# Kernel tuning notes

Hardware: AMD Instinct MI355X
Metric: run time of the kernel (lower is better)

## Reference

```python
import jax, jax.numpy as jnp
import numpy as np

N, E, F, H, C = 50000, 800000, 128, 256, 40
BN_EPS = 1e-5


def setup_inputs() -> dict:
    key = jax.random.key(0)
    ks = jax.random.split(key, 8)
    s = 0.05
    return {
        'x': jax.random.normal(ks[0], (N, F), jnp.float32),
        'edge_index': jax.random.randint(ks[1], (2, E), 0, N),
        'eps1': jnp.zeros((), jnp.float32),
        'W1': jax.random.normal(ks[2], (F, H), jnp.float32) * s,
        'b1': jnp.zeros((H,), jnp.float32),
        'g1': jnp.ones((H,), jnp.float32),
        'be1': jnp.zeros((H,), jnp.float32),
        'W2': jax.random.normal(ks[3], (H, H), jnp.float32) * s,
        'b2': jnp.zeros((H,), jnp.float32),
        'eps2': jnp.zeros((), jnp.float32),
        'W3': jax.random.normal(ks[4], (H, H), jnp.float32) * s,
        'b3': jnp.zeros((H,), jnp.float32),
        'g2': jnp.ones((H,), jnp.float32),
        'be2': jnp.zeros((H,), jnp.float32),
        'W4': jax.random.normal(ks[5], (H, H), jnp.float32) * s,
        'b4': jnp.zeros((H,), jnp.float32),
        'g3': jnp.ones((H,), jnp.float32),
        'be3': jnp.zeros((H,), jnp.float32),
        'Wf': jax.random.normal(ks[6], (H, C), jnp.float32) * s,
        'bf': jnp.zeros((C,), jnp.float32),
    }


def _bn(h, g, b):
    # BatchNorm1d forward with batch statistics (training-mode math, biased var)
    m = jnp.mean(h, axis=0)
    v = jnp.var(h, axis=0)
    return (h - m) * jax.lax.rsqrt(v + BN_EPS) * g + b


def _gin_conv(x, edge_index, eps, Wa, ba, g, be, Wb, bb):
    # GINConv: out = mlp((1+eps)*x + sum_{(src->dst)} x[src])
    src, dst = edge_index[0], edge_index[1]
    agg = jax.ops.segment_sum(x[src], dst, num_segments=x.shape[0])  # [N, d]
    h = (1.0 + eps) * x + agg
    h = jnp.maximum(_bn(h @ Wa + ba, g, be), 0.0)  # Linear-BN-ReLU
    return h @ Wb + bb                              # Linear


def reference(x, edge_index, eps1, W1, b1, g1, be1, W2, b2,
              eps2, W3, b3, g2, be2, W4, b4, g3, be3, Wf, bf):
    h = _gin_conv(x, edge_index, eps1, W1, b1, g1, be1, W2, b2)
    h = jnp.maximum(h, 0.0)  # F.relu (dropout p=0)
    h = _gin_conv(h, edge_index, eps2, W3, b3, g2, be2, W4, b4)
    h = jnp.maximum(_bn(h, g3, be3), 0.0)  # bn2 + relu
    return h @ Wf + bf  # fc -> [N, C]
```

## Files before the change

### kernel.cpp

```cpp
#include <hip/hip_runtime.h>
#include <hip/hip_bf16.h>


#define NN 50000
#define EE 800000
#define FDIM 128
#define HDIM 256
#define CDIM 40
#define BN_EPS 1e-5f
#define CSTRIDE 136

typedef unsigned short u16;
typedef unsigned int u32;
typedef __attribute__((ext_vector_type(8))) short short8;
typedef __attribute__((ext_vector_type(4))) float f32x4;

__device__ __forceinline__ float bflo(u32 u) { return __uint_as_float(u << 16); }
__device__ __forceinline__ float bfhi(u32 u) { return __uint_as_float(u & 0xFFFF0000u); }
__device__ __forceinline__ u16 f2bf(float f) {
  __hip_bfloat16 h = __float2bfloat16(f);
  return *(u16*)&h;
}
__device__ __forceinline__ u32 pack2(float a, float b) {
  return (u32)f2bf(a) | ((u32)f2bf(b) << 16);
}

__global__ void k_hist(const int* __restrict__ ei, int* __restrict__ deg) {
  int e = blockIdx.x * 256 + threadIdx.x;
  if (e < EE) atomicAdd(&deg[ei[EE + e]], 1);
}

__global__ void k_scan_blocks(const int* __restrict__ in, int* __restrict__ partial,
                              int* __restrict__ bsums, int n) {
  __shared__ int s[256];
  int i = blockIdx.x * 256 + threadIdx.x;
  s[threadIdx.x] = (i < n) ? in[i] : 0;
  __syncthreads();
  for (int d = 1; d < 256; d <<= 1) {
    int t = (threadIdx.x >= d) ? s[threadIdx.x - d] : 0;
    __syncthreads();
    s[threadIdx.x] += t;
    __syncthreads();
  }
  if (i < n) partial[i] = s[threadIdx.x];
  if (threadIdx.x == 255) bsums[blockIdx.x] = s[255];
}

__global__ void k_scan_sums(int* __restrict__ bs, int nb) {
  __shared__ int s[256];
  s[threadIdx.x] = (threadIdx.x < nb) ? bs[threadIdx.x] : 0;
  __syncthreads();
  for (int d = 1; d < 256; d <<= 1) {
    int t = (threadIdx.x >= d) ? s[threadIdx.x - d] : 0;
    __syncthreads();
    s[threadIdx.x] += t;
    __syncthreads();
  }
  int ex = (threadIdx.x == 0) ? 0 : s[threadIdx.x - 1];
  if (threadIdx.x < nb) bs[threadIdx.x] = ex;
}

__global__ void k_scan_add(const int* __restrict__ partial, const int* __restrict__ bs,
                           int* __restrict__ rowstart, int n) {
  int i = blockIdx.x * 256 + threadIdx.x;
  if (i < n) rowstart[i + 1] = partial[i] + bs[blockIdx.x];
  if (i == 0) rowstart[0] = 0;
}

__global__ void k_copy_i32(const int* __restrict__ a, int* __restrict__ b, int n) {
  int i = blockIdx.x * 256 + threadIdx.x;
  if (i < n) b[i] = a[i];
}

__global__ void k_scatter(const int* __restrict__ ei, int* __restrict__ cursor,
                          int* __restrict__ sorted_src) {
  int e = blockIdx.x * 256 + threadIdx.x;
  if (e < EE) {
    int dst = ei[EE + e];
    int p = atomicAdd(&cursor[dst], 1);
    sorted_src[p] = ei[e];
  }
}

__global__ void k_cvt_x(const float* __restrict__ x, u16* __restrict__ xb) {
  int i = blockIdx.x * 256 + threadIdx.x;
  size_t base = (size_t)i * 4;
  if (base < (size_t)NN * FDIM) {
    float4 v = *(const float4*)&x[base];
    u32 lo = pack2(v.x, v.y), hi = pack2(v.z, v.w);
    *(uint2*)&xb[base] = make_uint2(lo, hi);
  }
}

__global__ void k_cvt_wt(const float* __restrict__ W, u16* __restrict__ Wt, int K) {
  int i = blockIdx.x * 256 + threadIdx.x;
  int k = i >> 8, n = i & 255;
  if (k < K) Wt[(size_t)n * K + k] = f2bf(W[i]);
}

template <int FEAT>
__global__ __launch_bounds__(256)
void k_agg(const u16* __restrict__ x, const int* __restrict__ rowstart,
           const int* __restrict__ sorted_src, const float* __restrict__ epsp,
           u16* __restrict__ out) {
  int node = blockIdx.x * 4 + (threadIdx.x >> 6);
  if (node >= NN) return;
  int lane = threadIdx.x & 63;
  float e1 = 1.0f + epsp[0];
  int s = rowstart[node], t = rowstart[node + 1];
  if constexpr (FEAT == 128) {
    const u32* xp = (const u32*)x;
    u32 u = xp[(size_t)node * 64 + lane];
    float a0 = bflo(u) * e1, a1 = bfhi(u) * e1;
    int p = s;
    for (; p + 7 < t; p += 8) {
      u32 uu[8];
#pragma unroll
      for (int i = 0; i < 8; ++i) uu[i] = xp[(size_t)sorted_src[p + i] * 64 + lane];
#pragma unroll
      for (int i = 0; i < 8; ++i) { a0 += bflo(uu[i]); a1 += bfhi(uu[i]); }
    }
    for (; p + 1 < t; p += 2) {
      u32 u0 = xp[(size_t)sorted_src[p] * 64 + lane];
      u32 u1 = xp[(size_t)sorted_src[p + 1] * 64 + lane];
      a0 += bflo(u0) + bflo(u1);
      a1 += bfhi(u0) + bfhi(u1);
    }
    if (p < t) {
      u32 u0 = xp[(size_t)sorted_src[p] * 64 + lane];
      a0 += bflo(u0); a1 += bfhi(u0);
    }
    ((u32*)out)[(size_t)node * 64 + lane] = pack2(a0, a1);
  } else {
    const uint2* xp = (const uint2*)x;
    uint2 u = xp[(size_t)node * 64 + lane];
    float a0 = bflo(u.x) * e1, a1 = bfhi(u.x) * e1;
    float a2 = bflo(u.y) * e1, a3 = bfhi(u.y) * e1;
    int p = s;
    for (; p + 7 < t; p += 8) {
      uint2 uu[8];
#pragma unroll
      for (int i = 0; i < 8; ++i) uu[i] = xp[(size_t)sorted_src[p + i] * 64 + lane];
#pragma unroll
      for (int i = 0; i < 8; ++i) {
        a0 += bflo(uu[i].x); a1 += bfhi(uu[i].x);
        a2 += bflo(uu[i].y); a3 += bfhi(uu[i].y);
      }
    }
    for (; p + 1 < t; p += 2) {
      uint2 u0 = xp[(size_t)sorted_src[p] * 64 + lane];
      uint2 u1 = xp[(size_t)sorted_src[p + 1] * 64 + lane];
      a0 += bflo(u0.x) + bflo(u1.x);
      a1 += bfhi(u0.x) + bfhi(u1.x);
      a2 += bflo(u0.y) + bflo(u1.y);
      a3 += bfhi(u0.y) + bfhi(u1.y);
    }
    if (p < t) {
      uint2 u0 = xp[(size_t)sorted_src[p] * 64 + lane];
      a0 += bflo(u0.x); a1 += bfhi(u0.x);
      a2 += bflo(u0.y); a3 += bfhi(u0.y);
    }
    ((uint2*)out)[(size_t)node * 64 + lane] = make_uint2(pack2(a0, a1), pack2(a2, a3));
  }
}

template <int K, bool TRANSFORM, bool RELU_OUT, bool COLSUMS>
__global__ __launch_bounds__(256)
void k_gemm(const u16* __restrict__ A, const u16* __restrict__ Bt,
            const float* __restrict__ bias, const float* __restrict__ ta,
            const float* __restrict__ tc, u16* __restrict__ C,
            float* __restrict__ csum, float* __restrict__ csq) {
  constexpr int NCH = K / 8;
  constexpr int NKS = K / 32;
  constexpr int NTILE = (NN + 31) / 32;
  __shared__ u16 Bs[128 * K];
  __shared__ u16 Cs[32 * CSTRIDE];
  __shared__ float2 Tb[K];

  const int tid = threadIdx.x;
  const int lane = tid & 63;
  const int w = tid >> 6;
  const int wm = w >> 1, wn = w & 1;
  const int lr = lane & 15, lq = lane >> 4;
  const int half = blockIdx.x & 1;
  const u16* Bth = Bt + (size_t)half * 128 * K;

  for (int i = tid; i < 128 * NCH; i += 256) {
    int row = i / NCH, c = i % NCH;
    short8 v = *(const short8*)&Bth[(size_t)row * K + c * 8];
    ((short8*)Bs)[row * NCH + (c ^ (row & 7))] = v;
  }
  if constexpr (TRANSFORM) {
    for (int k = tid; k < K; k += 256) Tb[k] = make_float2(ta[k], tc[k]);
  }

  float bv[4];
#pragma unroll
  for (int ni = 0; ni < 4; ++ni) bv[ni] = bias[half * 128 + wn * 64 + ni * 16 + lr];
  float colS[4] = {}, colQ[4] = {};

  __syncthreads();

  short8 bufA[NKS], bufB[NKS];

  auto LOADA = [&](short8* dst, int rt) {
    int row = rt * 32 + wm * 16 + lr;
    int rowc = row < NN ? row : NN - 1;
    const u16* Ap = &A[(size_t)rowc * K];
#pragma unroll
    for (int ks = 0; ks < NKS; ++ks)
      dst[ks] = *(const short8*)&Ap[ks * 32 + lq * 8];
  };

  auto BODY = [&](short8* cur, short8* nxt, int rt) {
    if constexpr (TRANSFORM) {
#pragma unroll
      for (int ks = 0; ks < NKS; ++ks) {
        short8 v = cur[ks];
#pragma unroll
        for (int j = 0; j < 8; ++j) {
          float2 tb = Tb[ks * 32 + lq * 8 + j];
          float f = __uint_as_float(((u32)(u16)v[j]) << 16);
          v[j] = (short)f2bf(fmaxf(fmaf(f, tb.x, tb.y), 0.f));
        }
        cur[ks] = v;
      }
    }
    if (rt + 256 < NTILE) LOADA(nxt, rt + 256);

    f32x4 acc[4];
#pragma unroll
    for (int ni = 0; ni < 4; ++ni) acc[ni] = (f32x4){0.f, 0.f, 0.f, 0.f};
    __builtin_amdgcn_s_setprio(1);
#pragma unroll
    for (int ks = 0; ks < NKS; ++ks) {
#pragma unroll
      for (int ni = 0; ni < 4; ++ni) {
        int col = wn * 64 + ni * 16 + lr;
        int c = (ks * 4 + lq) ^ (col & 7);
        short8 bfr = ((const short8*)Bs)[col * NCH + c];
        acc[ni] = __builtin_amdgcn_mfma_f32_16x16x32_bf16(cur[ks], bfr, acc[ni], 0, 0, 0);
      }
    }
    __builtin_amdgcn_s_setprio(0);

#pragma unroll
    for (int ni = 0; ni < 4; ++ni) {
      int col = wn * 64 + ni * 16 + lr;
#pragma unroll
      for (int j = 0; j < 4; ++j) {
        int r = wm * 16 + lq * 4 + j;
        float v = acc[ni][j] + bv[ni];
        if constexpr (RELU_OUT) v = fmaxf(v, 0.f);
        if constexpr (COLSUMS) {
          if (rt * 32 + r < NN) { colS[ni] += v; colQ[ni] += v * v; }
        }
        Cs[r * CSTRIDE + col] = f2bf(v);
      }
    }
    __syncthreads();
    {
      int r = tid >> 3;
      int gr = rt * 32 + r;
      if (gr < NN) {
        const uint4* src = (const uint4*)&Cs[r * CSTRIDE + (tid & 7) * 16];
        uint4 v0 = src[0], v1 = src[1];
        uint4* dst = (uint4*)&C[(size_t)gr * HDIM + half * 128 + (tid & 7) * 16];
        dst[0] = v0; dst[1] = v1;
      }
    }
    __syncthreads();
  };

  LOADA(bufA, blockIdx.x >> 1);
  for (int rt = blockIdx.x >> 1; rt < NTILE; rt += 512) {
    BODY(bufA, bufB, rt);
    if (rt + 256 < NTILE) BODY(bufB, bufA, rt + 256);
  }

  if constexpr (COLSUMS) {
#pragma unroll
    for (int ni = 0; ni < 4; ++ni) {
      float s = colS[ni], q = colQ[ni];
      s += __shfl_xor(s, 16); s += __shfl_xor(s, 32);
      q += __shfl_xor(q, 16); q += __shfl_xor(q, 32);
      if (lq == 0) {
        int col = half * 128 + wn * 64 + ni * 16 + lr;
        atomicAdd(&csum[col], s);
        atomicAdd(&csq[col], q);
      }
    }
  }
}

__global__ void k_bn_fin(const float* __restrict__ sum, const float* __restrict__ sq,
                         const float* __restrict__ g, const float* __restrict__ be,
                         float* __restrict__ a, float* __restrict__ c) {
  int t = threadIdx.x;
  float m = sum[t] * (1.0f / NN);
  float var = sq[t] * (1.0f / NN) - m * m;
  float s = g[t] * rsqrtf(var + BN_EPS);
  a[t] = s;
  c[t] = be[t] - m * s;
}

__global__ __launch_bounds__(256)
void k_gemm_final(const u16* __restrict__ A, const float* __restrict__ B,
                  const float* __restrict__ bias, const float* __restrict__ ta,
                  const float* __restrict__ tc, float* __restrict__ C) {
  __shared__ float As[64][65];
  __shared__ float Bs[64][CDIM];
  int tid = threadIdx.x;
  int r = tid & 63, q = tid >> 6;
  int r0 = blockIdx.x * 64;
  float acc[10] = {};
  for (int k0 = 0; k0 < HDIM; k0 += 64) {
#pragma unroll
    for (int i = 0; i < 4; ++i) {
      int idx = tid + i * 256;
      int row = idx >> 4;
      int c4 = (idx & 15) * 4;
      int gr = r0 + row;
      float v0 = 0.f, v1 = 0.f, v2 = 0.f, v3 = 0.f;
      if (gr < NN) {
        uint2 u = *(const uint2*)&A[(size_t)gr * HDIM + k0 + c4];
        v0 = fmaxf(fmaf(bflo(u.x), ta[k0 + c4 + 0], tc[k0 + c4 + 0]), 0.f);
        v1 = fmaxf(fmaf(bfhi(u.x), ta[k0 + c4 + 1], tc[k0 + c4 + 1]), 0.f);
        v2 = fmaxf(fmaf(bflo(u.y), ta[k0 + c4 + 2], tc[k0 + c4 + 2]), 0.f);
        v3 = fmaxf(fmaf(bfhi(u.y), ta[k0 + c4 + 3], tc[k0 + c4 + 3]), 0.f);
      }
      As[c4 + 0][row] = v0;
      As[c4 + 1][row] = v1;
      As[c4 + 2][row] = v2;
      As[c4 + 3][row] = v3;
    }
#pragma unroll
    for (int i = 0; i < 10; ++i) {
      int idx = tid + i * 256;
      int row = idx / CDIM;
      int col = idx % CDIM;
      Bs[row][col] = B[(size_t)(k0 + row) * CDIM + col];
    }
    __syncthreads();
#pragma unroll
    for (int k = 0; k < 64; ++k) {
      float a = As[k][r];
#pragma unroll
      for (int j = 0; j < 10; ++j) acc[j] = fmaf(a, Bs[k][q * 10 + j], acc[j]);
    }
    __syncthreads();
  }
  int gr = r0 + r;
  if (gr < NN) {
#pragma unroll
    for (int j = 0; j < 10; ++j) C[(size_t)gr * CDIM + q * 10 + j] = acc[j] + bias[q * 10 + j];
  }
}

extern "C" void kernel_launch(void* const* d_in, const int* in_sizes, int n_in,
                              void* d_out, int out_size, void* d_ws, size_t ws_size,
                              hipStream_t stream) {
  const float* x   = (const float*)d_in[0];
  const int*   ei  = (const int*)d_in[1];
  const float* eps1= (const float*)d_in[2];
  const float* W1  = (const float*)d_in[3];
  const float* b1  = (const float*)d_in[4];
  const float* g1  = (const float*)d_in[5];
  const float* be1 = (const float*)d_in[6];
  const float* W2  = (const float*)d_in[7];
  const float* b2  = (const float*)d_in[8];
  const float* eps2= (const float*)d_in[9];
  const float* W3  = (const float*)d_in[10];
  const float* b3  = (const float*)d_in[11];
  const float* g2  = (const float*)d_in[12];
  const float* be2 = (const float*)d_in[13];
  const float* W4  = (const float*)d_in[14];
  const float* b4  = (const float*)d_in[15];
  const float* g3  = (const float*)d_in[16];
  const float* be3 = (const float*)d_in[17];
  const float* Wf  = (const float*)d_in[18];
  const float* bf  = (const float*)d_in[19];
  float* out = (float*)d_out;

  char* p = (char*)d_ws;
  auto alloc = [&](size_t bytes) -> char* {
    char* r = p;
    p += (bytes + 255) & ~(size_t)255;
    return r;
  };
  float* stats   = (float*)alloc(12 * 256 * sizeof(float));
  int* deg       = (int*)alloc(NN * sizeof(int));
  int* rowstart  = (int*)alloc((NN + 16) * sizeof(int));
  int* cursor    = (int*)alloc(NN * sizeof(int));
  int* sorted    = (int*)alloc(EE * sizeof(int));
  int* partial   = (int*)alloc(NN * sizeof(int));
  int* bsums     = (int*)alloc(1024 * sizeof(int));
  u16* W1t       = (u16*)alloc(256 * 128 * sizeof(u16));
  u16* W2t       = (u16*)alloc(256 * 256 * sizeof(u16));
  u16* W3t       = (u16*)alloc(256 * 256 * sizeof(u16));
  u16* W4t       = (u16*)alloc(256 * 256 * sizeof(u16));
  u16* xb        = (u16*)alloc((size_t)NN * 128 * sizeof(u16));
  u16* A1        = (u16*)alloc((size_t)NN * 128 * sizeof(u16));
  u16* z1        = (u16*)alloc((size_t)NN * 256 * sizeof(u16));
  u16* h1        = (u16*)alloc((size_t)NN * 256 * sizeof(u16));
  u16* A2        = (u16*)alloc((size_t)NN * 256 * sizeof(u16));
  (void)alloc(64 * 1024);
  u16* z2 = z1;
  u16* z3 = h1;

  hipMemsetAsync(deg, 0, NN * sizeof(int), stream);
  hipMemsetAsync(stats, 0, 12 * 256 * sizeof(float), stream);

  const int nbE = (EE + 255) / 256;
  const int nbN = (NN + 255) / 256;

  k_hist<<<nbE, 256, 0, stream>>>(ei, deg);
  k_scan_blocks<<<nbN, 256, 0, stream>>>(deg, partial, bsums, NN);
  k_scan_sums<<<1, 256, 0, stream>>>(bsums, nbN);
  k_scan_add<<<nbN, 256, 0, stream>>>(partial, bsums, rowstart, NN);
  k_copy_i32<<<nbN, 256, 0, stream>>>(rowstart, cursor, NN);
  k_scatter<<<nbE, 256, 0, stream>>>(ei, cursor, sorted);

  k_cvt_x<<<(NN * FDIM / 4 + 255) / 256, 256, 0, stream>>>(x, xb);
  k_cvt_wt<<<128, 256, 0, stream>>>(W1, W1t, 128);
  k_cvt_wt<<<256, 256, 0, stream>>>(W2, W2t, 256);
  k_cvt_wt<<<256, 256, 0, stream>>>(W3, W3t, 256);
  k_cvt_wt<<<256, 256, 0, stream>>>(W4, W4t, 256);

  k_agg<128><<<(NN + 3) / 4, 256, 0, stream>>>(xb, rowstart, sorted, eps1, A1);
  k_gemm<128, false, false, true><<<512, 256, 0, stream>>>(
      A1, W1t, b1, nullptr, nullptr, z1, stats + 0, stats + 256);
  k_bn_fin<<<1, 256, 0, stream>>>(stats + 0, stats + 256, g1, be1,
                                  stats + 2 * 256, stats + 3 * 256);
  k_gemm<256, true, true, false><<<512, 256, 0, stream>>>(
      z1, W2t, b2, stats + 2 * 256, stats + 3 * 256, h1, nullptr, nullptr);

  k_agg<256><<<(NN + 3) / 4, 256, 0, stream>>>(h1, rowstart, sorted, eps2, A2);
  k_gemm<256, false, false, true><<<512, 256, 0, stream>>>(
      A2, W3t, b3, nullptr, nullptr, z2, stats + 4 * 256, stats + 5 * 256);
  k_bn_fin<<<1, 256, 0, stream>>>(stats + 4 * 256, stats + 5 * 256, g2, be2,
                                  stats + 6 * 256, stats + 7 * 256);
  k_gemm<256, true, false, true><<<512, 256, 0, stream>>>(
      z2, W4t, b4, stats + 6 * 256, stats + 7 * 256, z3, stats + 8 * 256, stats + 9 * 256);
  k_bn_fin<<<1, 256, 0, stream>>>(stats + 8 * 256, stats + 9 * 256, g3, be3,
                                  stats + 10 * 256, stats + 11 * 256);

  k_gemm_final<<<(NN + 63) / 64, 256, 0, stream>>>(
      z3, Wf, bf, stats + 10 * 256, stats + 11 * 256, out);
}
```

Baseline: 391.4 us.

## Restructure GEMMs to full-width 64-row tiles, fuse BN finalize, use MFMA for final layer

```diff
diff --git a/kernel.cpp b/kernel.cpp
--- a/kernel.cpp
+++ b/kernel.cpp
@@ -8,7 +8,6 @@
 #define HDIM 256
 #define CDIM 40
 #define BN_EPS 1e-5f
-#define CSTRIDE 136
 
 typedef unsigned short u16;
 typedef unsigned int u32;
@@ -61,15 +60,15 @@
 }
 
 __global__ void k_scan_add(const int* __restrict__ partial, const int* __restrict__ bs,
-                           int* __restrict__ rowstart, int n) {
+                           const int* __restrict__ deg,
+                           int* __restrict__ rowstart, int* __restrict__ cursor, int n) {
   int i = blockIdx.x * 256 + threadIdx.x;
-  if (i < n) rowstart[i + 1] = partial[i] + bs[blockIdx.x];
+  if (i < n) {
+    int incl = partial[i] + bs[blockIdx.x];
+    rowstart[i + 1] = incl;
+    cursor[i] = incl - deg[i];
+  }
   if (i == 0) rowstart[0] = 0;
-}
-
-__global__ void k_copy_i32(const int* __restrict__ a, int* __restrict__ b, int n) {
-  int i = blockIdx.x * 256 + threadIdx.x;
-  if (i < n) b[i] = a[i];
 }
 
 __global__ void k_scatter(const int* __restrict__ ei, int* __restrict__ cursor,
@@ -82,20 +81,43 @@
   }
 }
 
-__global__ void k_cvt_x(const float* __restrict__ x, u16* __restrict__ xb) {
+__global__ void k_cvt_x(const float* __restrict__ x, u16* __restrict__ xb,
+                        int* __restrict__ deg, float* __restrict__ stats) {
   int i = blockIdx.x * 256 + threadIdx.x;
+  if (i < NN) deg[i] = 0;
+  if (i < 6 * 256) stats[i] = 0.f;
   size_t base = (size_t)i * 4;
   if (base < (size_t)NN * FDIM) {
     float4 v = *(const float4*)&x[base];
-    u32 lo = pack2(v.x, v.y), hi = pack2(v.z, v.w);
-    *(uint2*)&xb[base] = make_uint2(lo, hi);
-  }
-}
-
-__global__ void k_cvt_wt(const float* __restrict__ W, u16* __restrict__ Wt, int K) {
-  int i = blockIdx.x * 256 + threadIdx.x;
-  int k = i >> 8, n = i & 255;
-  if (k < K) Wt[(size_t)n * K + k] = f2bf(W[i]);
+    *(uint2*)&xb[base] = make_uint2(pack2(v.x, v.y), pack2(v.z, v.w));
+  }
+}
+
+__global__ void k_cvt_w(const float* __restrict__ W1, const float* __restrict__ W2,
+                        const float* __restrict__ W3, const float* __restrict__ W4,
+                        const float* __restrict__ Wf,
+                        u16* __restrict__ W1t, u16* __restrict__ W2t,
+                        u16* __restrict__ W3t, u16* __restrict__ W4t,
+                        u16* __restrict__ Wft) {
+  int b = blockIdx.x, t = threadIdx.x;
+  if (b < 128) {
+    int i = b * 256 + t; int k = i >> 8, n = i & 255;
+    W1t[(size_t)n * 128 + (((k >> 3) ^ (n & 7)) << 3) + (k & 7)] = f2bf(W1[i]);
+  } else if (b < 384) {
+    int i = (b - 128) * 256 + t; int k = i >> 8, n = i & 255;
+    W2t[(size_t)n * 256 + (((k >> 3) ^ (n & 7)) << 3) + (k & 7)] = f2bf(W2[i]);
+  } else if (b < 640) {
+    int i = (b - 384) * 256 + t; int k = i >> 8, n = i & 255;
+    W3t[(size_t)n * 256 + (((k >> 3) ^ (n & 7)) << 3) + (k & 7)] = f2bf(W3[i]);
+  } else if (b < 896) {
+    int i = (b - 640) * 256 + t; int k = i >> 8, n = i & 255;
+    W4t[(size_t)n * 256 + (((k >> 3) ^ (n & 7)) << 3) + (k & 7)] = f2bf(W4[i]);
+  } else {
+    int j = (b - 896) * 256 + t;
+    int c = j >> 8, k = j & 255;
+    float v = (c < CDIM) ? Wf[(size_t)k * CDIM + c] : 0.f;
+    Wft[(size_t)c * 256 + (((k >> 3) ^ (c & 7)) << 3) + (k & 7)] = f2bf(v);
+  }
 }
 
 template <int FEAT>
@@ -165,117 +187,120 @@
 }
 
 template <int K, bool TRANSFORM, bool RELU_OUT, bool COLSUMS>
-__global__ __launch_bounds__(256)
+__global__ __launch_bounds__(512)
 void k_gemm(const u16* __restrict__ A, const u16* __restrict__ Bt,
-            const float* __restrict__ bias, const float* __restrict__ ta,
-            const float* __restrict__ tc, u16* __restrict__ C,
-            float* __restrict__ csum, float* __restrict__ csq) {
-  constexpr int NCH = K / 8;
+            const float* __restrict__ bias,
+            const float* __restrict__ icsum, const float* __restrict__ icsq,
+            const float* __restrict__ g, const float* __restrict__ be,
+            u16* __restrict__ C, float* __restrict__ ocsum, float* __restrict__ ocsq) {
   constexpr int NKS = K / 32;
-  constexpr int NTILE = (NN + 31) / 32;
-  __shared__ u16 Bs[128 * K];
-  __shared__ u16 Cs[32 * CSTRIDE];
-  __shared__ float2 Tb[K];
+  __shared__ u16 Bs[256 * K];
+  __shared__ u16 Cs[32 * 256];
+  __shared__ float2 Tb[TRANSFORM ? K : 1];
 
   const int tid = threadIdx.x;
   const int lane = tid & 63;
   const int w = tid >> 6;
-  const int wm = w >> 1, wn = w & 1;
+  const int wm = w >> 2, wn = w & 3;
   const int lr = lane & 15, lq = lane >> 4;
-  const int half = blockIdx.x & 1;
-  const u16* Bth = Bt + (size_t)half * 128 * K;
-
-  for (int i = tid; i < 128 * NCH; i += 256) {
-    int row = i / NCH, c = i % NCH;
-    short8 v = *(const short8*)&Bth[(size_t)row * K + c * 8];
-    ((short8*)Bs)[row * NCH + (c ^ (row & 7))] = v;
+  const int r0 = blockIdx.x * 64;
+
+  short8 a[2][NKS];
+#pragma unroll
+  for (int mi = 0; mi < 2; ++mi) {
+    int row = r0 + wm * 32 + mi * 16 + lr;
+    int rc = row < NN ? row : NN - 1;
+    const u16* Ap = &A[(size_t)rc * K];
+#pragma unroll
+    for (int ks = 0; ks < NKS; ++ks)
+      a[mi][ks] = *(const short8*)&Ap[(ks * 4 + lq) * 8];
+  }
+
+  {
+    const short8* Bv = (const short8*)Bt;
+    short8* Bl = (short8*)Bs;
+#pragma unroll
+    for (int i = 0; i < K / 16; ++i)
+      Bl[tid + i * 512] = Bv[tid + i * 512];
   }
   if constexpr (TRANSFORM) {
-    for (int k = tid; k < K; k += 256) Tb[k] = make_float2(ta[k], tc[k]);
-  }
-
-  float bv[4];
-#pragma unroll
-  for (int ni = 0; ni < 4; ++ni) bv[ni] = bias[half * 128 + wn * 64 + ni * 16 + lr];
-  float colS[4] = {}, colQ[4] = {};
-
+    if (tid < 256) {
+      float m = icsum[tid] * (1.0f / NN);
+      float var = icsq[tid] * (1.0f / NN) - m * m;
+      float s = g[tid] * rsqrtf(var + BN_EPS);
+      Tb[tid] = make_float2(s, be[tid] - m * s);
+    }
+  }
   __syncthreads();
 
-  short8 bufA[NKS], bufB[NKS];
-
-  auto LOADA = [&](short8* dst, int rt) {
-    int row = rt * 32 + wm * 16 + lr;
-    int rowc = row < NN ? row : NN - 1;
-    const u16* Ap = &A[(size_t)rowc * K];
-#pragma unroll
-    for (int ks = 0; ks < NKS; ++ks)
-      dst[ks] = *(const short8*)&Ap[ks * 32 + lq * 8];
-  };
-
-  auto BODY = [&](short8* cur, short8* nxt, int rt) {
+  f32x4 acc[2][4];
+#pragma unroll
+  for (int mi = 0; mi < 2; ++mi)
+#pragma unroll
+    for (int ni = 0; ni < 4; ++ni) acc[mi][ni] = (f32x4){0.f, 0.f, 0.f, 0.f};
+
+#pragma unroll
+  for (int ks = 0; ks < NKS; ++ks) {
+    short8 am0, am1;
     if constexpr (TRANSFORM) {
-#pragma unroll
-      for (int ks = 0; ks < NKS; ++ks) {
-        short8 v = cur[ks];
-#pragma unroll
-        for (int j = 0; j < 8; ++j) {
-          float2 tb = Tb[ks * 32 + lq * 8 + j];
-          float f = __uint_as_float(((u32)(u16)v[j]) << 16);
-          v[j] = (short)f2bf(fmaxf(fmaf(f, tb.x, tb.y), 0.f));
-        }
-        cur[ks] = v;
+      short8 t0 = a[0][ks], t1 = a[1][ks];
+      int kb = (ks * 4 + lq) * 8;
+#pragma unroll
+      for (int j = 0; j < 8; ++j) {
+        float2 tb = Tb[kb + j];
+        float f0 = fmaxf(fmaf(__uint_as_float(((u32)(u16)t0[j]) << 16), tb.x, tb.y), 0.f);
+        float f1 = fmaxf(fmaf(__uint_as_float(((u32)(u16)t1[j]) << 16), tb.x, tb.y), 0.f);
+        t0[j] = (short)f2bf(f0);
+        t1[j] = (short)f2bf(f1);
       }
-    }
-    if (rt + 256 < NTILE) LOADA(nxt, rt + 256);
-
-    f32x4 acc[4];
-#pragma unroll
-    for (int ni = 0; ni < 4; ++ni) acc[ni] = (f32x4){0.f, 0.f, 0.f, 0.f};
-    __builtin_amdgcn_s_setprio(1);
-#pragma unroll
-    for (int ks = 0; ks < NKS; ++ks) {
-#pragma unroll
-      for (int ni = 0; ni < 4; ++ni) {
-        int col = wn * 64 + ni * 16 + lr;
-        int c = (ks * 4 + lq) ^ (col & 7);
-        short8 bfr = ((const short8*)Bs)[col * NCH + c];
-        acc[ni] = __builtin_amdgcn_mfma_f32_16x16x32_bf16(cur[ks], bfr, acc[ni], 0, 0, 0);
-      }
-    }
-    __builtin_amdgcn_s_setprio(0);
-
+      am0 = t0; am1 = t1;
+    } else {
+      am0 = a[0][ks]; am1 = a[1][ks];
+    }
 #pragma unroll
     for (int ni = 0; ni < 4; ++ni) {
       int col = wn * 64 + ni * 16 + lr;
-#pragma unroll
-      for (int j = 0; j < 4; ++j) {
-        int r = wm * 16 + lq * 4 + j;
-        float v = acc[ni][j] + bv[ni];
-        if constexpr (RELU_OUT) v = fmaxf(v, 0.f);
-        if constexpr (COLSUMS) {
-          if (rt * 32 + r < NN) { colS[ni] += v; colQ[ni] += v * v; }
+      short8 bfr = *(const short8*)&Bs[(size_t)col * K + (((ks * 4 + lq) ^ (col & 7)) << 3)];
+      acc[0][ni] = __builtin_amdgcn_mfma_f32_16x16x32_bf16(am0, bfr, acc[0][ni], 0, 0, 0);
+      acc[1][ni] = __builtin_amdgcn_mfma_f32_16x16x32_bf16(am1, bfr, acc[1][ni], 0, 0, 0);
+    }
+  }
+
+  float bv[4];
+#pragma unroll
+  for (int ni = 0; ni < 4; ++ni) bv[ni] = bias[wn * 64 + ni * 16 + lr];
+  float colS[4] = {}, colQ[4] = {};
+
+#pragma unroll
+  for (int r = 0; r < 2; ++r) {
+    if (wm == r) {
+#pragma unroll
+      for (int mi = 0; mi < 2; ++mi)
+#pragma unroll
+        for (int ni = 0; ni < 4; ++ni) {
+          int col = wn * 64 + ni * 16 + lr;
+#pragma unroll
+          for (int j = 0; j < 4; ++j) {
+            int lrow = mi * 16 + lq * 4 + j;
+            float v = acc[mi][ni][j] + bv[ni];
+            if constexpr (RELU_OUT) v = fmaxf(v, 0.f);
+            if constexpr (COLSUMS) {
+              if (r0 + r * 32 + lrow < NN) { colS[ni] += v; colQ[ni] += v * v; }
+            }
+            Cs[lrow * 256 + col] = f2bf(v);
+          }
         }
-        Cs[r * CSTRIDE + col] = f2bf(v);
-      }
-    }
-    __syncthreads();
-    {
-      int r = tid >> 3;
-      int gr = rt * 32 + r;
-      if (gr < NN) {
-        const uint4* src = (const uint4*)&Cs[r * CSTRIDE + (tid & 7) * 16];
-        uint4 v0 = src[0], v1 = src[1];
-        uint4* dst = (uint4*)&C[(size_t)gr * HDIM + half * 128 + (tid & 7) * 16];
-        dst[0] = v0; dst[1] = v1;
-      }
-    }
-    __syncthreads();
-  };
-
-  LOADA(bufA, blockIdx.x >> 1);
-  for (int rt = blockIdx.x >> 1; rt < NTILE; rt += 512) {
-    BODY(bufA, bufB, rt);
-    if (rt + 256 < NTILE) BODY(bufB, bufA, rt + 256);
+    }
+    __syncthreads();
+#pragma unroll
+    for (int sub = 0; sub < 2; ++sub) {
+      int lrow = sub * 16 + (tid >> 5);
+      int gr = r0 + r * 32 + lrow;
+      if (gr < NN)
+        *(uint4*)&C[(size_t)gr * 256 + (tid & 31) * 8] =
+            *(const uint4*)&Cs[lrow * 256 + (tid & 31) * 8];
+    }
+    __syncthreads();
   }
 
   if constexpr (COLSUMS) {
@@ -285,75 +310,83 @@
       s += __shfl_xor(s, 16); s += __shfl_xor(s, 32);
       q += __shfl_xor(q, 16); q += __shfl_xor(q, 32);
       if (lq == 0) {
-        int col = half * 128 + wn * 64 + ni * 16 + lr;
-        atomicAdd(&csum[col], s);
-        atomicAdd(&csq[col], q);
+        int col = wn * 64 + ni * 16 + lr;
+        atomicAdd(&ocsum[col], s);
+        atomicAdd(&ocsq[col], q);
       }
     }
   }
 }
 
-__global__ void k_bn_fin(const float* __restrict__ sum, const float* __restrict__ sq,
-                         const float* __restrict__ g, const float* __restrict__ be,
-                         float* __restrict__ a, float* __restrict__ c) {
-  int t = threadIdx.x;
-  float m = sum[t] * (1.0f / NN);
-  float var = sq[t] * (1.0f / NN) - m * m;
-  float s = g[t] * rsqrtf(var + BN_EPS);
-  a[t] = s;
-  c[t] = be[t] - m * s;
-}
-
-__global__ __launch_bounds__(256)
-void k_gemm_final(const u16* __restrict__ A, const float* __restrict__ B,
-                  const float* __restrict__ bias, const float* __restrict__ ta,
-                  const float* __restrict__ tc, float* __restrict__ C) {
-  __shared__ float As[64][65];
-  __shared__ float Bs[64][CDIM];
-  int tid = threadIdx.x;
-  int r = tid & 63, q = tid >> 6;
-  int r0 = blockIdx.x * 64;
-  float acc[10] = {};
-  for (int k0 = 0; k0 < HDIM; k0 += 64) {
-#pragma unroll
-    for (int i = 0; i < 4; ++i) {
-      int idx = tid + i * 256;
-      int row = idx >> 4;
-      int c4 = (idx & 15) * 4;
-      int gr = r0 + row;
-      float v0 = 0.f, v1 = 0.f, v2 = 0.f, v3 = 0.f;
-      if (gr < NN) {
-        uint2 u = *(const uint2*)&A[(size_t)gr * HDIM + k0 + c4];
-        v0 = fmaxf(fmaf(bflo(u.x), ta[k0 + c4 + 0], tc[k0 + c4 + 0]), 0.f);
-        v1 = fmaxf(fmaf(bfhi(u.x), ta[k0 + c4 + 1], tc[k0 + c4 + 1]), 0.f);
-        v2 = fmaxf(fmaf(bflo(u.y), ta[k0 + c4 + 2], tc[k0 + c4 + 2]), 0.f);
-        v3 = fmaxf(fmaf(bfhi(u.y), ta[k0 + c4 + 3], tc[k0 + c4 + 3]), 0.f);
+__global__ __launch_bounds__(512)
+void k_final(const u16* __restrict__ z3, const u16* __restrict__ Wft,
+             const float* __restrict__ bfp,
+             const float* __restrict__ icsum, const float* __restrict__ icsq,
+             const float* __restrict__ g, const float* __restrict__ be,
+             float* __restrict__ out) {
+  __shared__ u16 Bs[48 * 256];
+  __shared__ float2 Tb[256];
+  const int tid = threadIdx.x;
+  const int lane = tid & 63;
+  const int w = tid >> 6;
+  const int lr = lane & 15, lq = lane >> 4;
+  const int r0 = blockIdx.x * 128;
+
+  int row = r0 + w * 16 + lr;
+  int rc = row < NN ? row : NN - 1;
+  const u16* Ap = &z3[(size_t)rc * 256];
+  short8 a[8];
+#pragma unroll
+  for (int ks = 0; ks < 8; ++ks)
+    a[ks] = *(const short8*)&Ap[(ks * 4 + lq) * 8];
+
+  {
+    const short8* Bv = (const short8*)Wft;
+    short8* Bl = (short8*)Bs;
+#pragma unroll
+    for (int i = 0; i < 3; ++i)
+      Bl[tid + i * 512] = Bv[tid + i * 512];
+  }
+  if (tid < 256) {
+    float m = icsum[tid] * (1.0f / NN);
+    float var = icsq[tid] * (1.0f / NN) - m * m;
+    float s = g[tid] * rsqrtf(var + BN_EPS);
+    Tb[tid] = make_float2(s, be[tid] - m * s);
+  }
+  __syncthreads();
+
+  f32x4 acc[3];
+#pragma unroll
+  for (int ni = 0; ni < 3; ++ni) acc[ni] = (f32x4){0.f, 0.f, 0.f, 0.f};
+#pragma unroll
+  for (int ks = 0; ks < 8; ++ks) {
+    short8 t0 = a[ks];
+    int kb = (ks * 4 + lq) * 8;
+#pragma unroll
+    for (int j = 0; j < 8; ++j) {
+      float2 tb = Tb[kb + j];
+      float f0 = fmaxf(fmaf(__uint_as_float(((u32)(u16)t0[j]) << 16), tb.x, tb.y), 0.f);
+      t0[j] = (short)f2bf(f0);
+    }
+#pragma unroll
+    for (int ni = 0; ni < 3; ++ni) {
+      int col = ni * 16 + lr;
+      short8 bfr = *(const short8*)&Bs[(size_t)col * 256 + (((ks * 4 + lq) ^ (col & 7)) << 3)];
+      acc[ni] = __builtin_amdgcn_mfma_f32_16x16x32_bf16(t0, bfr, acc[ni], 0, 0, 0);
+    }
+  }
+
+#pragma unroll
+  for (int ni = 0; ni < 3; ++ni) {
+    int col = ni * 16 + lr;
+    if (col < CDIM) {
+      float bfv = bfp[col];
+#pragma unroll
+      for (int j = 0; j < 4; ++j) {
+        int gr = r0 + w * 16 + lq * 4 + j;
+        if (gr < NN) out[(size_t)gr * CDIM + col] = acc[ni][j] + bfv;
       }
-      As[c4 + 0][row] = v0;
-      As[c4 + 1][row] = v1;
-      As[c4 + 2][row] = v2;
-      As[c4 + 3][row] = v3;
-    }
-#pragma unroll
-    for (int i = 0; i < 10; ++i) {
-      int idx = tid + i * 256;
-      int row = idx / CDIM;
-      int col = idx % CDIM;
-      Bs[row][col] = B[(size_t)(k0 + row) * CDIM + col];
-    }
-    __syncthreads();
-#pragma unroll
-    for (int k = 0; k < 64; ++k) {
-      float a = As[k][r];
-#pragma unroll
-      for (int j = 0; j < 10; ++j) acc[j] = fmaf(a, Bs[k][q * 10 + j], acc[j]);
-    }
-    __syncthreads();
-  }
-  int gr = r0 + r;
-  if (gr < NN) {
-#pragma unroll
-    for (int j = 0; j < 10; ++j) C[(size_t)gr * CDIM + q * 10 + j] = acc[j] + bias[q * 10 + j];
+    }
   }
 }
 
@@ -388,7 +421,7 @@
     p += (bytes + 255) & ~(size_t)255;
     return r;
   };
-  float* stats   = (float*)alloc(12 * 256 * sizeof(float));
+  float* stats   = (float*)alloc(6 * 256 * sizeof(float));
   int* deg       = (int*)alloc(NN * sizeof(int));
   int* rowstart  = (int*)alloc((NN + 16) * sizeof(int));
   int* cursor    = (int*)alloc(NN * sizeof(int));
@@ -399,6 +432,7 @@
   u16* W2t       = (u16*)alloc(256 * 256 * sizeof(u16));
   u16* W3t       = (u16*)alloc(256 * 256 * sizeof(u16));
   u16* W4t       = (u16*)alloc(256 * 256 * sizeof(u16));
+  u16* Wft       = (u16*)alloc(48 * 256 * sizeof(u16));
   u16* xb        = (u16*)alloc((size_t)NN * 128 * sizeof(u16));
   u16* A1        = (u16*)alloc((size_t)NN * 128 * sizeof(u16));
   u16* z1        = (u16*)alloc((size_t)NN * 256 * sizeof(u16));
@@ -408,43 +442,34 @@
   u16* z2 = z1;
   u16* z3 = h1;
 
-  hipMemsetAsync(deg, 0, NN * sizeof(int), stream);
-  hipMemsetAsync(stats, 0, 12 * 256 * sizeof(float), stream);
+  float* s1 = stats + 0,    *q1 = stats + 256;
+  float* s2 = stats + 512,  *q2 = stats + 768;
+  float* s3 = stats + 1024, *q3 = stats + 1280;
 
   const int nbE = (EE + 255) / 256;
   const int nbN = (NN + 255) / 256;
 
+  k_cvt_x<<<(NN * FDIM / 4 + 255) / 256, 256, 0, stream>>>(x, xb, deg, stats);
+  k_cvt_w<<<944, 256, 0, stream>>>(W1, W2, W3, W4, Wf, W1t, W2t, W3t, W4t, Wft);
   k_hist<<<nbE, 256, 0, stream>>>(ei, deg);
   k_scan_blocks<<<nbN, 256, 0, stream>>>(deg, partial, bsums, NN);
   k_scan_sums<<<1, 256, 0, stream>>>(bsums, nbN);
-  k_scan_add<<<nbN, 256, 0, stream>>>(partial, bsums, rowstart, NN);
-  k_copy_i32<<<nbN, 256, 0, stream>>>(rowstart, cursor, NN);
+  k_scan_add<<<nbN, 256, 0, stream>>>(partial, bsums, deg, rowstart, cursor, NN);
   k_scatter<<<nbE, 256, 0, stream>>>(ei, cursor, sorted);
 
-  k_cvt_x<<<(NN * FDIM / 4 + 255) / 256, 256, 0, stream>>>(x, xb);
-  k_cvt_wt<<<128, 256, 0, stream>>>(W1, W1t, 128);
-  k_cvt_wt<<<256, 256, 0, stream>>>(W2, W2t, 256);
-  k_cvt_wt<<<256, 256, 0, stream>>>(W3, W3t, 256);
-  k_cvt_wt<<<256, 256, 0, stream>>>(W4, W4t, 256);
+  const int gGemm = (NN + 63) / 64;
 
   k_agg<128><<<(NN + 3) / 4, 256, 0, stream>>>(xb, rowstart, sorted, eps1, A1);
-  k_gemm<128, false, false, true><<<512, 256, 0, stream>>>(
-      A1, W1t, b1, nullptr, nullptr, z1, stats + 0, stats + 256);
-  k_bn_fin<<<1, 256, 0, stream>>>(stats + 0, stats + 256, g1, be1,
-                                  stats + 2 * 256, stats + 3 * 256);
-  k_gemm<256, true, true, false><<<512, 256, 0, stream>>>(
-      z1, W2t, b2, stats + 2 * 256, stats + 3 * 256, h1, nullptr, nullptr);
+  k_gemm<128, false, false, true><<<gGemm, 512, 0, stream>>>(
+      A1, W1t, b1, nullptr, nullptr, nullptr, nullptr, z1, s1, q1);
+  k_gemm<256, true, true, false><<<gGemm, 512, 0, stream>>>(
+      z1, W2t, b2, s1, q1, g1, be1, h1, nullptr, nullptr);
 
   k_agg<256><<<(NN + 3) / 4, 256, 0, stream>>>(h1, rowstart, sorted, eps2, A2);
-  k_gemm<256, false, false, true><<<512, 256, 0, stream>>>(
-      A2, W3t, b3, nullptr, nullptr, z2, stats + 4 * 256, stats + 5 * 256);
-  k_bn_fin<<<1, 256, 0, stream>>>(stats + 4 * 256, stats + 5 * 256, g2, be2,
-                                  stats + 6 * 256, stats + 7 * 256);
-  k_gemm<256, true, false, true><<<512, 256, 0, stream>>>(
-      z2, W4t, b4, stats + 6 * 256, stats + 7 * 256, z3, stats + 8 * 256, stats + 9 * 256);
-  k_bn_fin<<<1, 256, 0, stream>>>(stats + 8 * 256, stats + 9 * 256, g3, be3,
-                                  stats + 10 * 256, stats + 11 * 256);
-
-  k_gemm_final<<<(NN + 63) / 64, 256, 0, stream>>>(
-      z3, Wf, bf, stats + 10 * 256, stats + 11 * 256, out);
-}
+  k_gemm<256, false, false, true><<<gGemm, 512, 0, stream>>>(
+      A2, W3t, b3, nullptr, nullptr, nullptr, nullptr, z2, s2, q2);
+  k_gemm<256, true, false, true><<<gGemm, 512, 0, stream>>>(
+      z2, W4t, b4, s2, q2, g2, be2, z3, s3, q3);
+
+  k_final<<<(NN + 127) / 128, 512, 0, stream>>>(z3, Wft, bf, s3, q3, g3, be3, out);
+}
```

Result: slower. 411.3 us (+5.1%).
